# Kernel tuning notes

Hardware: AMD Instinct MI355X
Metric: run time of the kernel (lower is better)

The kernel has to match this reference:

```python
import jax, jax.numpy as jnp
import numpy as np

N_NODES = 100000
N_EDGES = 1200000
D_NODE = 64
D_EDGE = 64
HIDDEN = 128
EPS = 1e-5


def setup_inputs() -> dict:
    key = jax.random.key(0)
    ks = jax.random.split(key, 10)
    d_in = D_NODE + D_EDGE  # 128
    s0 = 1.0 / np.sqrt(d_in)
    s1 = 1.0 / np.sqrt(HIDDEN)
    return {
        "x": jax.random.normal(ks[0], (N_NODES, D_NODE), dtype=jnp.float32),
        "edge_index": jax.random.randint(ks[1], (2, N_EDGES), 0, N_NODES, dtype=jnp.int64),
        "edge_attr": jax.random.normal(ks[2], (N_EDGES, D_EDGE), dtype=jnp.float32),
        # MLP params: Linear(d_in,H) -> ReLU -> Linear(H,H) -> ReLU -> Linear(H,D_NODE) -> LayerNorm
        "W0": jax.random.uniform(ks[3], (d_in, HIDDEN), jnp.float32, -s0, s0),
        "b0": jnp.zeros((HIDDEN,), jnp.float32),
        "W1": jax.random.uniform(ks[4], (HIDDEN, HIDDEN), jnp.float32, -s1, s1),
        "b1": jnp.zeros((HIDDEN,), jnp.float32),
        "W2": jax.random.uniform(ks[5], (HIDDEN, D_NODE), jnp.float32, -s1, s1),
        "b2": jnp.zeros((D_NODE,), jnp.float32),
        "ln_g": jnp.ones((D_NODE,), jnp.float32),
        "ln_b": jnp.zeros((D_NODE,), jnp.float32),
    }


def _layer_norm(h, g, b):
    mu = jnp.mean(h, axis=-1, keepdims=True)
    var = jnp.mean(jnp.square(h - mu), axis=-1, keepdims=True)
    return (h - mu) * jax.lax.rsqrt(var + EPS) * g + b


def reference(x, edge_index, edge_attr, W0, b0, W1, b1, W2, b2, ln_g, ln_b):
    col = edge_index[1]
    # scatter_sum(edge_attr, col, dim=0): segment sum over destination nodes -> [N, D_EDGE]
    agg = jax.ops.segment_sum(edge_attr, col, num_segments=N_NODES)
    h = jnp.concatenate([x, agg], axis=-1)  # [N, D_NODE + D_EDGE]
    h = jax.nn.relu(h @ W0 + b0)
    h = jax.nn.relu(h @ W1 + b1)
    h = h @ W2 + b2
    h = _layer_norm(h, ln_g, ln_b)
    return h + x
```

## Files before the change

kernel.cpp:

```cpp
#include <hip/hip_runtime.h>

#define NNODES 100000
#define DN 64
#define SROW 136

typedef short bf16x8 __attribute__((ext_vector_type(8)));
typedef float f32x4 __attribute__((ext_vector_type(4)));

__device__ __forceinline__ unsigned short f2bf(float f) {
  unsigned int u = __float_as_uint(f);
  u = (u + 0x7fffu + ((u >> 16) & 1u)) >> 16;
  return (unsigned short)u;
}

__global__ __launch_bounds__(256) void hist_kernel(const int* __restrict__ col,
                                                   int* __restrict__ deg, int n) {
  int i = blockIdx.x * 256 + threadIdx.x;
  if (i < n) atomicAdd(&deg[col[i]], 1);
}

__global__ __launch_bounds__(1024) void scan_blk(const int* __restrict__ deg,
                                                 int* __restrict__ bsum) {
  __shared__ int red[1024];
  int t = threadIdx.x;
  int i = blockIdx.x * 1024 + t;
  red[t] = (i < NNODES) ? deg[i] : 0;
  __syncthreads();
  for (int off = 512; off > 0; off >>= 1) {
    if (t < off) red[t] += red[t + off];
    __syncthreads();
  }
  if (t == 0) bsum[blockIdx.x] = red[0];
}

__global__ __launch_bounds__(128) void scan_top(int* __restrict__ bsum) {
  __shared__ int tmp[128];
  int t = threadIdx.x;
  if (t < 98) tmp[t] = bsum[t];
  __syncthreads();
  if (t == 0) {
    int run = 0;
    for (int i = 0; i < 98; ++i) { int v = tmp[i]; tmp[i] = run; run += v; }
  }
  __syncthreads();
  if (t < 98) bsum[t] = tmp[t];
}

__global__ __launch_bounds__(1024) void scan_fin(const int* __restrict__ deg,
                                                 const int* __restrict__ bsum,
                                                 int* __restrict__ row_ptr,
                                                 int* __restrict__ cursor) {
  __shared__ int ps[1024];
  int t = threadIdx.x;
  int i = blockIdx.x * 1024 + t;
  int v = (i < NNODES) ? deg[i] : 0;
  ps[t] = v;
  __syncthreads();
  for (int off = 1; off < 1024; off <<= 1) {
    int u = (t >= off) ? ps[t - off] : 0;
    __syncthreads();
    ps[t] += u;
    __syncthreads();
  }
  int excl = ps[t] - v + bsum[blockIdx.x];
  if (i < NNODES) { row_ptr[i] = excl; cursor[i] = excl; }
  if (i == NNODES - 1) row_ptr[NNODES] = excl + v;
}

__global__ __launch_bounds__(256) void fill_kernel(const int* __restrict__ col,
                                                   int* __restrict__ cursor,
                                                   int* __restrict__ elist, int n) {
  int i = blockIdx.x * 256 + threadIdx.x;
  if (i < n) {
    int pos = atomicAdd(&cursor[col[i]], 1);
    elist[pos] = i;
  }
}

__global__ __launch_bounds__(256) void gather_kernel(
    const int* __restrict__ row_ptr, const int* __restrict__ elist,
    const float* __restrict__ ea, unsigned short* __restrict__ aggb) {
  const int wid = threadIdx.x >> 6;
  const int lane = threadIdx.x & 63;
  const int node = blockIdx.x * 4 + wid;
  if (node >= NNODES) return;
  const int s = row_ptr[node], e = row_ptr[node + 1];
  const int g = lane >> 4;
  const int c4 = (lane & 15) * 4;
  float ax = 0.f, ay = 0.f, az = 0.f, aw = 0.f;
  for (int i = s + g; i < e; i += 4) {
    int ed = elist[i];
    const float4 v = *(const float4*)(ea + (size_t)ed * 64 + c4);
    ax += v.x; ay += v.y; az += v.z; aw += v.w;
  }
  ax += __shfl_xor(ax, 16); ay += __shfl_xor(ay, 16);
  az += __shfl_xor(az, 16); aw += __shfl_xor(aw, 16);
  ax += __shfl_xor(ax, 32); ay += __shfl_xor(ay, 32);
  az += __shfl_xor(az, 32); aw += __shfl_xor(aw, 32);
  if (g == 0) {
    ushort4 o;
    o.x = f2bf(ax); o.y = f2bf(ay); o.z = f2bf(az); o.w = f2bf(aw);
    *(ushort4*)(aggb + (size_t)node * 64 + c4) = o;
  }
}

__global__ __launch_bounds__(256) void wprep_kernel(
    const float* __restrict__ W0, const float* __restrict__ W1,
    const float* __restrict__ W2, unsigned short* __restrict__ wp) {
  int t = blockIdx.x * 256 + threadIdx.x;
  if (t >= 5120) return;
  const float* W; int c, N, dstbase;
  if (t < 2048)      { W = W0; c = t;        N = 128; dstbase = 0; }
  else if (t < 4096) { W = W1; c = t - 2048; N = 128; dstbase = 16384; }
  else               { W = W2; c = t - 4096; N = 64;  dstbase = 32768; }
  int blk = c >> 6;
  int lane = c & 63;
  int nc = blk >> 2, kc = blk & 3;
  int k0 = kc * 32 + (lane >> 4) * 8;
  int n  = nc * 16 + (lane & 15);
  unsigned short* dst = wp + dstbase + blk * 512 + lane * 8;
#pragma unroll
  for (int j = 0; j < 8; ++j) dst[j] = f2bf(W[(size_t)(k0 + j) * N + n]);
}

__global__ __launch_bounds__(256) void fused_mlp(
    const float* __restrict__ x, const unsigned short* __restrict__ aggb,
    const unsigned short* __restrict__ wp,
    const float* __restrict__ b0, const float* __restrict__ b1,
    const float* __restrict__ b2, const float* __restrict__ lng,
    const float* __restrict__ lnb, float* __restrict__ out) {
  __shared__ unsigned short act[4 * 2 * 16 * SROW];

  const int tid = threadIdx.x;
  const int wid = tid >> 6;
  const int lane = tid & 63;
  const int gw = blockIdx.x * 4 + wid;
  if (gw >= NNODES / 16) return;
  const int base = gw * 16;
  const int m = lane & 15;
  const int quad = lane >> 4;

  unsigned short* Abuf = act + (wid * 2 + 0) * 16 * SROW;
  unsigned short* Bbuf = act + (wid * 2 + 1) * 16 * SROW;

#pragma unroll 4
  for (int r = 0; r < 16; ++r) {
    int node = base + r;
    Abuf[r * SROW + lane] = f2bf(x[(size_t)node * 64 + lane]);
    Abuf[r * SROW + 64 + lane] = aggb[(size_t)node * 64 + lane];
  }

  bf16x8 af[4];

#pragma unroll
  for (int kc = 0; kc < 4; ++kc)
    af[kc] = *(const bf16x8*)(Abuf + m * SROW + kc * 32 + quad * 8);
#pragma unroll
  for (int nc = 0; nc < 8; ++nc) {
    float bv = b0[nc * 16 + m];
    f32x4 acc = {bv, bv, bv, bv};
#pragma unroll
    for (int kc = 0; kc < 4; ++kc) {
      bf16x8 bf = *(const bf16x8*)(wp + (nc * 4 + kc) * 512 + lane * 8);
      acc = __builtin_amdgcn_mfma_f32_16x16x32_bf16(af[kc], bf, acc, 0, 0, 0);
    }
    int col = nc * 16 + m;
#pragma unroll
    for (int r2 = 0; r2 < 4; ++r2)
      Bbuf[(quad * 4 + r2) * SROW + col] = f2bf(fmaxf(acc[r2], 0.f));
  }

#pragma unroll
  for (int kc = 0; kc < 4; ++kc)
    af[kc] = *(const bf16x8*)(Bbuf + m * SROW + kc * 32 + quad * 8);
#pragma unroll
  for (int nc = 0; nc < 8; ++nc) {
    float bv = b1[nc * 16 + m];
    f32x4 acc = {bv, bv, bv, bv};
#pragma unroll
    for (int kc = 0; kc < 4; ++kc) {
      bf16x8 bf = *(const bf16x8*)(wp + 16384 + (nc * 4 + kc) * 512 + lane * 8);
      acc = __builtin_amdgcn_mfma_f32_16x16x32_bf16(af[kc], bf, acc, 0, 0, 0);
    }
    int col = nc * 16 + m;
#pragma unroll
    for (int r2 = 0; r2 < 4; ++r2)
      Abuf[(quad * 4 + r2) * SROW + col] = f2bf(fmaxf(acc[r2], 0.f));
  }

#pragma unroll
  for (int kc = 0; kc < 4; ++kc)
    af[kc] = *(const bf16x8*)(Abuf + m * SROW + kc * 32 + quad * 8);
  f32x4 acc2[4];
#pragma unroll
  for (int nc = 0; nc < 4; ++nc) {
    float bv = b2[nc * 16 + m];
    f32x4 acc = {bv, bv, bv, bv};
#pragma unroll
    for (int kc = 0; kc < 4; ++kc) {
      bf16x8 bf = *(const bf16x8*)(wp + 32768 + (nc * 4 + kc) * 512 + lane * 8);
      acc = __builtin_amdgcn_mfma_f32_16x16x32_bf16(af[kc], bf, acc, 0, 0, 0);
    }
    acc2[nc] = acc;
  }

  float s[4], ss[4];
#pragma unroll
  for (int r2 = 0; r2 < 4; ++r2) {
    float a0 = acc2[0][r2], a1 = acc2[1][r2], a2 = acc2[2][r2], a3 = acc2[3][r2];
    s[r2]  = a0 + a1 + a2 + a3;
    ss[r2] = a0 * a0 + a1 * a1 + a2 * a2 + a3 * a3;
  }
#pragma unroll
  for (int msk = 1; msk < 16; msk <<= 1) {
#pragma unroll
    for (int r2 = 0; r2 < 4; ++r2) {
      s[r2]  += __shfl_xor(s[r2], msk);
      ss[r2] += __shfl_xor(ss[r2], msk);
    }
  }
  float mu[4], rs[4];
#pragma unroll
  for (int r2 = 0; r2 < 4; ++r2) {
    mu[r2] = s[r2] * 0.015625f;
    float var = ss[r2] * 0.015625f - mu[r2] * mu[r2];
    rs[r2] = rsqrtf(var + 1e-5f);
  }
#pragma unroll
  for (int nc = 0; nc < 4; ++nc) {
    int col = nc * 16 + m;
    float g = lng[col], bb = lnb[col];
#pragma unroll
    for (int r2 = 0; r2 < 4; ++r2) {
      int node = base + quad * 4 + r2;
      float xr = x[(size_t)node * 64 + col];
      out[(size_t)node * 64 + col] =
          (acc2[nc][r2] - mu[r2]) * rs[r2] * g + bb + xr;
    }
  }
}

extern "C" void kernel_launch(void* const* d_in, const int* in_sizes, int n_in,
                              void* d_out, int out_size, void* d_ws, size_t ws_size,
                              hipStream_t stream) {
  const float* x  = (const float*)d_in[0];
  const int*   ei = (const int*)d_in[1];
  const float* ea = (const float*)d_in[2];
  const float* W0 = (const float*)d_in[3];
  const float* b0 = (const float*)d_in[4];
  const float* W1 = (const float*)d_in[5];
  const float* b1 = (const float*)d_in[6];
  const float* W2 = (const float*)d_in[7];
  const float* b2 = (const float*)d_in[8];
  const float* lg = (const float*)d_in[9];
  const float* lb = (const float*)d_in[10];
  float* out = (float*)d_out;

  const int n_edges = in_sizes[2] / DN;
  const int* col = ei + n_edges;

  char* ws = (char*)d_ws;
  int* deg     = (int*)(ws + 0);
  int* row_ptr = (int*)(ws + 400000);
  int* cursor  = (int*)(ws + 800016);
  int* elist   = (int*)(ws + 1200016);
  unsigned short* wp = (unsigned short*)(ws + 6000016);
  int* bsum    = (int*)(ws + 6082000);
  unsigned short* aggb = (unsigned short*)(ws + 6082512);

  hipMemsetAsync(deg, 0, NNODES * sizeof(int), stream);

  hist_kernel<<<(n_edges + 255) / 256, 256, 0, stream>>>(col, deg, n_edges);
  scan_blk<<<98, 1024, 0, stream>>>(deg, bsum);
  scan_top<<<1, 128, 0, stream>>>(bsum);
  scan_fin<<<98, 1024, 0, stream>>>(deg, bsum, row_ptr, cursor);
  fill_kernel<<<(n_edges + 255) / 256, 256, 0, stream>>>(col, cursor, elist, n_edges);
  wprep_kernel<<<20, 256, 0, stream>>>(W0, W1, W2, wp);

  gather_kernel<<<(NNODES + 3) / 4, 256, 0, stream>>>(row_ptr, elist, ea, aggb);

  int nblocks = (NNODES / 16 + 3) / 4;
  fused_mlp<<<nblocks, 256, 0, stream>>>(x, aggb, wp, b0, b1, b2, lg, lb, out);
}
```

Baseline: 643.8 us.

## Scatter edge features into destination-sorted bf16 buffer before segment gather

The fill pass now reads every edge's fp32 feature row coalesced, converts it to bf16, and writes it into a destination-sorted buffer at the atomically claimed slot. The gather kernel then streams contiguous bf16 rows per node instead of doing random fp32 row reads through an edge index list. This swaps one random 256-byte read per edge for a coalesced read plus a scattered 128-byte write and a sequential read. Rounding each edge to bf16 before summing adds precision error.

```diff
diff --git a/kernel.cpp b/kernel.cpp
--- a/kernel.cpp
+++ b/kernel.cpp
@@ -11,6 +11,9 @@
   unsigned int u = __float_as_uint(f);
   u = (u + 0x7fffu + ((u >> 16) & 1u)) >> 16;
   return (unsigned short)u;
+}
+__device__ __forceinline__ float bf2f(unsigned short h) {
+  return __uint_as_float(((unsigned int)h) << 16);
 }
 
 __global__ __launch_bounds__(256) void hist_kernel(const int* __restrict__ col,
@@ -67,40 +70,50 @@
   if (i == NNODES - 1) row_ptr[NNODES] = excl + v;
 }
 
-__global__ __launch_bounds__(256) void fill_kernel(const int* __restrict__ col,
-                                                   int* __restrict__ cursor,
-                                                   int* __restrict__ elist, int n) {
-  int i = blockIdx.x * 256 + threadIdx.x;
-  if (i < n) {
-    int pos = atomicAdd(&cursor[col[i]], 1);
-    elist[pos] = i;
-  }
+__global__ __launch_bounds__(256) void fillconv_kernel(
+    const int* __restrict__ col, const float* __restrict__ ea,
+    int* __restrict__ cursor, unsigned short* __restrict__ sorted, int n) {
+  int t = blockIdx.x * 256 + threadIdx.x;
+  int e = t >> 4;
+  if (e >= n) return;
+  const int sub = t & 15;
+  const int lane = threadIdx.x & 63;
+  int d = col[e];
+  int pos = 0;
+  if (sub == 0) pos = atomicAdd(&cursor[d], 1);
+  pos = __shfl(pos, lane & 48);
+  float4 v = *(const float4*)(ea + (size_t)e * 64 + sub * 4);
+  ushort4 o;
+  o.x = f2bf(v.x); o.y = f2bf(v.y); o.z = f2bf(v.z); o.w = f2bf(v.w);
+  *(ushort4*)(sorted + (size_t)pos * 64 + sub * 4) = o;
 }
 
 __global__ __launch_bounds__(256) void gather_kernel(
-    const int* __restrict__ row_ptr, const int* __restrict__ elist,
-    const float* __restrict__ ea, unsigned short* __restrict__ aggb) {
+    const int* __restrict__ row_ptr, const unsigned short* __restrict__ sorted,
+    unsigned short* __restrict__ aggb) {
   const int wid = threadIdx.x >> 6;
   const int lane = threadIdx.x & 63;
   const int node = blockIdx.x * 4 + wid;
   if (node >= NNODES) return;
   const int s = row_ptr[node], e = row_ptr[node + 1];
-  const int g = lane >> 4;
-  const int c4 = (lane & 15) * 4;
-  float ax = 0.f, ay = 0.f, az = 0.f, aw = 0.f;
-  for (int i = s + g; i < e; i += 4) {
-    int ed = elist[i];
-    const float4 v = *(const float4*)(ea + (size_t)ed * 64 + c4);
-    ax += v.x; ay += v.y; az += v.z; aw += v.w;
-  }
-  ax += __shfl_xor(ax, 16); ay += __shfl_xor(ay, 16);
-  az += __shfl_xor(az, 16); aw += __shfl_xor(aw, 16);
-  ax += __shfl_xor(ax, 32); ay += __shfl_xor(ay, 32);
-  az += __shfl_xor(az, 32); aw += __shfl_xor(aw, 32);
-  if (g == 0) {
-    ushort4 o;
-    o.x = f2bf(ax); o.y = f2bf(ay); o.z = f2bf(az); o.w = f2bf(aw);
-    *(ushort4*)(aggb + (size_t)node * 64 + c4) = o;
+  const int ch0 = (lane & 7) * 8;
+  float acc[8];
+#pragma unroll
+  for (int k = 0; k < 8; ++k) acc[k] = 0.f;
+  for (int j = s + (lane >> 3); j < e; j += 8) {
+    bf16x8 v = *(const bf16x8*)(sorted + (size_t)j * 64 + ch0);
+#pragma unroll
+    for (int k = 0; k < 8; ++k) acc[k] += bf2f((unsigned short)v[k]);
+  }
+#pragma unroll
+  for (int msk = 8; msk < 64; msk <<= 1)
+#pragma unroll
+    for (int k = 0; k < 8; ++k) acc[k] += __shfl_xor(acc[k], msk);
+  if (lane < 8) {
+    bf16x8 o;
+#pragma unroll
+    for (int k = 0; k < 8; ++k) o[k] = (short)f2bf(acc[k]);
+    *(bf16x8*)(aggb + (size_t)node * 64 + lane * 8) = o;
   }
 }
 
@@ -263,10 +276,10 @@
   int* deg     = (int*)(ws + 0);
   int* row_ptr = (int*)(ws + 400000);
   int* cursor  = (int*)(ws + 800016);
-  int* elist   = (int*)(ws + 1200016);
-  unsigned short* wp = (unsigned short*)(ws + 6000016);
-  int* bsum    = (int*)(ws + 6082000);
-  unsigned short* aggb = (unsigned short*)(ws + 6082512);
+  int* bsum    = (int*)(ws + 1200016);
+  unsigned short* wp   = (unsigned short*)(ws + 1200512);
+  unsigned short* aggb = (unsigned short*)(ws + 1282432);
+  unsigned short* sorted = (unsigned short*)(ws + 14083072);
 
   hipMemsetAsync(deg, 0, NNODES * sizeof(int), stream);
 
@@ -274,10 +287,12 @@
   scan_blk<<<98, 1024, 0, stream>>>(deg, bsum);
   scan_top<<<1, 128, 0, stream>>>(bsum);
   scan_fin<<<98, 1024, 0, stream>>>(deg, bsum, row_ptr, cursor);
-  fill_kernel<<<(n_edges + 255) / 256, 256, 0, stream>>>(col, cursor, elist, n_edges);
   wprep_kernel<<<20, 256, 0, stream>>>(W0, W1, W2, wp);
 
-  gather_kernel<<<(NNODES + 3) / 4, 256, 0, stream>>>(row_ptr, elist, ea, aggb);
+  fillconv_kernel<<<(n_edges * 16 + 255) / 256, 256, 0, stream>>>(
+      col, ea, cursor, sorted, n_edges);
+
+  gather_kernel<<<(NNODES + 3) / 4, 256, 0, stream>>>(row_ptr, sorted, aggb);
 
   int nblocks = (NNODES / 16 + 3) / 4;
   fused_mlp<<<nblocks, 256, 0, stream>>>(x, aggb, wp, b0, b1, b2, lg, lb, out);
```

Result: faster. 584.0 us (-9.3%).
